# Kernel tuning notes

Hardware: AMD Instinct MI355X
Metric: run time of the kernel (lower is better)

## Reference

```python
import jax, jax.numpy as jnp
import numpy as np
import math

B, T, H, NH, L = 8, 256, 128, 2, 2
DH = H // NH
KC = 3
ITEMNUM = 50000
TIME_SPAN = 256
PERIODS = jnp.array([86400.0, 604800.0, 2592000.0], dtype=jnp.float32)
SCALE_MAGS = [1.0, 1.0, 1.0]
NEG = -1e9


def layernorm(x, g, b, eps=1e-8):
    mu = x.mean(-1, keepdims=True)
    var = ((x - mu) ** 2).mean(-1, keepdims=True)
    return (x - mu) / jnp.sqrt(var + eps) * g + b


def time_encode(t, time_proj):
    # HarmonicTimeEncoding: [sin(2*pi*t/c), cos(2*pi*t/c)] per cycle -> Linear(2K->H, no bias)
    phase = 2.0 * math.pi * t[..., None] / PERIODS
    enc = jnp.concatenate([jnp.sin(phase), jnp.cos(phase)], axis=-1)  # (..., 2K)
    return enc @ time_proj.T


def phase_bias_fn(t, lambdas):
    # PhaseSimilarityBias: per-cycle cosine similarity of (sin,cos) phase vectors
    phase = 2.0 * math.pi * t[..., None] / PERIODS  # (B,T,K)
    phi = jnp.stack([jnp.sin(phase), jnp.cos(phase)], axis=-1)  # (B,T,K,2)
    phi = phi / jnp.maximum(jnp.linalg.norm(phi, axis=-1, keepdims=True), 1e-12)
    sim = jnp.einsum('btkd,bskd->btsk', phi, phi)
    return (sim * lambdas).sum(-1)  # (B,T,T)


def setup_inputs() -> dict:
    key = jax.random.key(0)
    ks = jax.random.split(key, 40)
    def n(i, shape, std=0.02):
        return jax.random.normal(ks[i], shape, dtype=jnp.float32) * std
    inp = {}
    inp['log_seqs'] = jax.random.randint(ks[0], (B, T), 0, ITEMNUM + 1)
    inp['time_matrices'] = jax.random.randint(ks[1], (B, T, T), 0, TIME_SPAN + 1)
    inp['time_seq'] = jnp.sort(jax.random.uniform(ks[2], (B, T), dtype=jnp.float32) * 5e6, axis=-1)
    inp['pos_seqs'] = jax.random.randint(ks[3], (B, T), 1, ITEMNUM + 1)
    inp['neg_seqs'] = jax.random.randint(ks[4], (B, T), 1, ITEMNUM + 1)
    inp['target_times'] = jax.random.uniform(ks[5], (B,), dtype=jnp.float32) * 5e6
    inp['item_emb'] = n(6, (ITEMNUM + 1, H)).at[0].set(0.0)  # padding_idx=0
    inp['abs_pos_K'] = n(7, (T, H))
    inp['abs_pos_V'] = n(8, (T, H))
    inp['time_K_emb'] = n(9, (TIME_SPAN + 1, H))
    inp['time_V_emb'] = n(10, (TIME_SPAN + 1, H))
    inp['Wq'] = n(11, (L, H, H), 0.05); inp['bq'] = jnp.zeros((L, H))
    inp['Wk'] = n(12, (L, H, H), 0.05); inp['bk'] = jnp.zeros((L, H))
    inp['Wv'] = n(13, (L, H, H), 0.05); inp['bv'] = jnp.zeros((L, H))
    inp['attn_ln_g'] = jnp.ones((L, H)); inp['attn_ln_b'] = jnp.zeros((L, H))
    inp['fwd_ln_g'] = jnp.ones((L, H)); inp['fwd_ln_b'] = jnp.zeros((L, H))
    inp['w1'] = n(14, (L, H, H), 0.05); inp['b1'] = jnp.zeros((L, H))
    inp['w2'] = n(15, (L, H, H), 0.05); inp['b2'] = jnp.zeros((L, H))
    inp['last_ln_g'] = jnp.ones((H,)); inp['last_ln_b'] = jnp.zeros((H,))
    inp['time_proj'] = n(16, (H, 2 * KC), 1.0 / math.sqrt(H))
    inp['lambdas'] = jnp.array(SCALE_MAGS, dtype=jnp.float32)
    inp['pred_W'] = n(17, (H, H), 0.05)
    inp['fus_W1'] = n(18, (H, 2 * H), 0.05); inp['fus_b1'] = jnp.zeros((H,))
    inp['fus_W2'] = n(19, (H, H), 0.05); inp['fus_b2'] = jnp.zeros((H,))
    return inp


def reference(log_seqs, time_matrices, time_seq, pos_seqs, neg_seqs, target_times,
              item_emb, abs_pos_K, abs_pos_V, time_K_emb, time_V_emb,
              Wq, bq, Wk, bk, Wv, bv, attn_ln_g, attn_ln_b, fwd_ln_g, fwd_ln_b,
              w1, b1, w2, b2, last_ln_g, last_ln_b, time_proj, lambdas,
              pred_W, fus_W1, fus_b1, fus_W2, fus_b2):
    seqs = item_emb[log_seqs] * math.sqrt(H)
    seqs = seqs + time_encode(time_seq, time_proj)
    tl_mask = (log_seqs == 0)  # (B,T) padding mask
    keep = (~tl_mask)[..., None].astype(seqs.dtype)
    seqs = seqs * keep
    absK = abs_pos_K.reshape(T, NH, DH).transpose(1, 0, 2)  # (NH,T,DH)
    absV = abs_pos_V.reshape(T, NH, DH).transpose(1, 0, 2)
    tK = time_K_emb[time_matrices].reshape(B, T, T, NH, DH)  # (B,T,T,NH,DH)
    tV = time_V_emb[time_matrices].reshape(B, T, T, NH, DH)
    pbias = phase_bias_fn(time_seq, lambdas)  # (B,T,T)
    causal = jnp.triu(jnp.ones((T, T), dtype=bool), k=1)
    mask = causal[None, None] | tl_mask[:, None, None, :]  # (B,1,T,T)
    for l in range(L):
        Qn = layernorm(seqs, attn_ln_g[l], attn_ln_b[l])
        q = (Qn @ Wq[l].T + bq[l]).reshape(B, T, NH, DH).transpose(0, 2, 1, 3)
        k = (seqs @ Wk[l].T + bk[l]).reshape(B, T, NH, DH).transpose(0, 2, 1, 3)
        v = (seqs @ Wv[l].T + bv[l]).reshape(B, T, NH, DH).transpose(0, 2, 1, 3)
        scores = jnp.einsum('bhqd,bhkd->bhqk', q, k)
        scores = scores + jnp.einsum('bhqd,hkd->bhqk', q, absK)
        scores = scores + jnp.einsum('bqkhd,bhqd->bhqk', tK, q)  # relative time-interval term
        scores = scores / math.sqrt(DH) + pbias[:, None]  # phase-similarity logit bias
        scores = jnp.where(mask, NEG, scores)
        A = jax.nn.softmax(scores, axis=-1)
        out = jnp.einsum('bhqk,bhkd->bhqd', A, v)
        out = out + jnp.einsum('bhqk,hkd->bhqd', A, absV)
        out = out + jnp.einsum('bhqk,bqkhd->bhqd', A, tV)
        out = out.transpose(0, 2, 1, 3).reshape(B, T, H)
        seqs = Qn + out
        x = layernorm(seqs, fwd_ln_g[l], fwd_ln_b[l])
        seqs = jax.nn.relu(x @ w1[l].T + b1[l]) @ w2[l].T + b2[l] + x
        seqs = seqs * keep
    log_feats = layernorm(seqs, last_ln_g, last_ln_b)
    H_per = time_encode(target_times, time_proj) @ pred_W.T  # (B,H)
    H_per = jnp.broadcast_to(H_per[:, None], (B, T, H))
    cat = jnp.concatenate([log_feats, H_per], axis=-1)
    fused = jax.nn.gelu(cat @ fus_W1.T + fus_b1, approximate=False) @ fus_W2.T + fus_b2
    pos_logits = (fused * item_emb[pos_seqs]).sum(-1)
    neg_logits = (fused * item_emb[neg_seqs]).sum(-1)
    return (pos_logits, neg_logits)
```

## Files before the change

kernel.cpp:

```cpp
#include <hip/hip_runtime.h>
#include <math.h>

#define TT 256
#define HH 128

__device__ __forceinline__ void enc6(float t, float e[6]) {
  float x = 6.2831853071795864769f * t;
  float a0 = x / 86400.0f, a1 = x / 604800.0f, a2 = x / 2592000.0f;
  e[0] = sinf(a0); e[1] = sinf(a1); e[2] = sinf(a2);
  e[3] = cosf(a0); e[4] = cosf(a1); e[5] = cosf(a2);
}

__global__ __launch_bounds__(128) void embed_kernel(
    const int* __restrict__ log_seqs, const float* __restrict__ time_seq,
    const float* __restrict__ item_emb, const float* __restrict__ time_proj,
    float* __restrict__ seqs, float* __restrict__ sc6) {
  int row = blockIdx.x;
  int h = threadIdx.x;
  float t = time_seq[row];
  float e[6]; enc6(t, e);
  int idx = log_seqs[row];
  const float* tp = time_proj + h * 6;
  float val = item_emb[(size_t)idx * HH + h] * 11.313708498984761f;
  val += e[0]*tp[0] + e[1]*tp[1] + e[2]*tp[2] + e[3]*tp[3] + e[4]*tp[4] + e[5]*tp[5];
  seqs[(size_t)row * HH + h] = (idx != 0) ? val : 0.0f;
  if (h < 6) sc6[row * 6 + h] = e[h];
}

__global__ __launch_bounds__(128) void qkv_fused(
    const float* __restrict__ S,
    const float* __restrict__ Wq, const float* __restrict__ bq,
    const float* __restrict__ Wk, const float* __restrict__ bk,
    const float* __restrict__ Wv, const float* __restrict__ bv,
    const float* __restrict__ lng, const float* __restrict__ lnb,
    const float* __restrict__ absK, const float* __restrict__ absV,
    float* __restrict__ QN, float* __restrict__ QB,
    float* __restrict__ KT, float* __restrict__ VB) {
  int which = blockIdx.x >> 8;
  int m0 = (blockIdx.x & 255) * 8;
  int n = threadIdx.x;
  __shared__ float At[8][132];
  __shared__ float mu[8], rs[8];
  #pragma unroll
  for (int r = 0; r < 8; ++r) At[r][n] = S[(size_t)(m0 + r) * HH + n];
  __syncthreads();
  if (which == 0) {
    if (n < 64) {
      int r = n >> 3, sg = n & 7;
      float s = 0.f;
      #pragma unroll
      for (int i = 0; i < 16; ++i) s += At[r][sg * 16 + i];
      s += __shfl_xor(s, 1); s += __shfl_xor(s, 2); s += __shfl_xor(s, 4);
      if (sg == 0) mu[r] = s * (1.0f / HH);
    }
    __syncthreads();
    if (n < 64) {
      int r = n >> 3, sg = n & 7;
      float mm = mu[r], s = 0.f;
      #pragma unroll
      for (int i = 0; i < 16; ++i) { float d = At[r][sg*16+i] - mm; s += d * d; }
      s += __shfl_xor(s, 1); s += __shfl_xor(s, 2); s += __shfl_xor(s, 4);
      if (sg == 0) rs[r] = rsqrtf(s * (1.0f / HH) + 1e-8f);
    }
    __syncthreads();
    float gg = lng[n], bb = lnb[n];
    #pragma unroll
    for (int r = 0; r < 8; ++r) {
      float v = (At[r][n] - mu[r]) * rs[r] * gg + bb;
      At[r][n] = v;
      QN[(size_t)(m0 + r) * HH + n] = v;
    }
    __syncthreads();
  }
  const float* W    = which == 0 ? Wq : which == 1 ? Wk : Wv;
  const float* bias = which == 0 ? bq : which == 1 ? bk : bv;
  const float* addP = which == 1 ? absK : which == 2 ? absV : nullptr;
  float* dst        = which == 0 ? QB : which == 1 ? KT : VB;
  float acc[8];
  #pragma unroll
  for (int r = 0; r < 8; ++r) acc[r] = 0.f;
  const float* wr = W + (size_t)n * HH;
  for (int d = 0; d < HH; d += 4) {
    float4 w = *(const float4*)(wr + d);
    #pragma unroll
    for (int r = 0; r < 8; ++r) {
      float4 a = *(const float4*)(&At[r][d]);
      acc[r] = fmaf(a.x, w.x, fmaf(a.y, w.y, fmaf(a.z, w.z, fmaf(a.w, w.w, acc[r]))));
    }
  }
  float bn = bias[n];
  #pragma unroll
  for (int r = 0; r < 8; ++r) {
    int m = m0 + r;
    float v = acc[r] + bn;
    if (addP) v += addP[(size_t)(m & 255) * HH + n];
    if (which == 1) {
      int bb2 = m >> 8, t = m & 255, hh2 = n >> 6, dd = n & 63;
      dst[(((size_t)(bb2 * 2 + hh2) * 64) + dd) * 256 + t] = v;
    } else {
      dst[(size_t)m * HH + n] = v;
    }
  }
}

__global__ __launch_bounds__(256) void pkscb_kernel(
    const float* __restrict__ QB, const float* __restrict__ tKe,
    const int* __restrict__ tmat, const int* __restrict__ log_seqs,
    const float* __restrict__ sc6, const float* __restrict__ lambdas,
    float* __restrict__ SCB) {
  int blk = blockIdx.x;
  int qt = blk & 63, bh = blk >> 6;
  int h = bh & 1, b = bh >> 1;
  int q0 = qt << 2, hoff = h << 6;
  int tid = threadIdx.x;
  __shared__ float Qs[4][64];
  __shared__ float PKl[4][264];
  __shared__ float sk6T[6][256];
  __shared__ float sq6[4][6];
  __shared__ unsigned char kmask[256];
  { int q = tid >> 6, d = tid & 63;
    Qs[q][d] = QB[((size_t)(b * TT + q0 + q)) * HH + hoff + d]; }
  for (int idx = tid; idx < 1536; idx += 256) {
    int kk = idx / 6, cc = idx - kk * 6;
    sk6T[cc][kk] = sc6[(size_t)b * 1536 + idx];
  }
  if (tid < 24) {
    int q = tid / 6, cc = tid - q * 6;
    sq6[q][cc] = sc6[((size_t)(b * TT + q0 + q)) * 6 + cc];
  }
  kmask[tid] = (log_seqs[b * TT + tid] == 0) ? 1 : 0;
  __syncthreads();
  for (int i = tid; i < 257; i += 256) {
    const float* tp = tKe + (size_t)i * HH + hoff;
    float a0 = 0.f, a1 = 0.f, a2 = 0.f, a3 = 0.f;
    #pragma unroll
    for (int d = 0; d < 64; d += 4) {
      float4 t4 = *(const float4*)(tp + d);
      float4 v0 = *(const float4*)(&Qs[0][d]);
      float4 v1 = *(const float4*)(&Qs[1][d]);
      float4 v2 = *(const float4*)(&Qs[2][d]);
      float4 v3 = *(const float4*)(&Qs[3][d]);
      a0 = fmaf(v0.x,t4.x,fmaf(v0.y,t4.y,fmaf(v0.z,t4.z,fmaf(v0.w,t4.w,a0))));
      a1 = fmaf(v1.x,t4.x,fmaf(v1.y,t4.y,fmaf(v1.z,t4.z,fmaf(v1.w,t4.w,a1))));
      a2 = fmaf(v2.x,t4.x,fmaf(v2.y,t4.y,fmaf(v2.z,t4.z,fmaf(v2.w,t4.w,a2))));
      a3 = fmaf(v3.x,t4.x,fmaf(v3.y,t4.y,fmaf(v3.z,t4.z,fmaf(v3.w,t4.w,a3))));
    }
    PKl[0][i] = a0 * 0.125f; PKl[1][i] = a1 * 0.125f;
    PKl[2][i] = a2 * 0.125f; PKl[3][i] = a3 * 0.125f;
  }
  __syncthreads();
  float l0 = lambdas[0], l1 = lambdas[1], l2 = lambdas[2];
  int k = tid;
  float c0 = sk6T[0][k], c1 = sk6T[1][k], c2 = sk6T[2][k],
        c3 = sk6T[3][k], c4 = sk6T[4][k], c5 = sk6T[5][k];
  int km = kmask[k];
  float* scbq = SCB + ((size_t)(bh * TT + q0)) * TT;
  #pragma unroll
  for (int qq = 0; qq < 4; ++qq) {
    int qg = q0 + qq;
    float pb = l0 * (sq6[qq][0] * c0 + sq6[qq][3] * c3)
             + l1 * (sq6[qq][1] * c1 + sq6[qq][4] * c4)
             + l2 * (sq6[qq][2] * c2 + sq6[qq][5] * c5);
    int tm = tmat[((size_t)(b * TT + qg)) * TT + k];
    float val = (k > qg || km) ? -1e9f : (PKl[qq][tm] + pb);
    scbq[(size_t)qq * TT + k] = val;
  }
}

__global__ __launch_bounds__(256) void attn_fused(
    const float* __restrict__ QB, const float* __restrict__ KT,
    const float* __restrict__ VB, const float* __restrict__ QN,
    const float* __restrict__ SCB, const int* __restrict__ tmat,
    const float* __restrict__ tVe, float* __restrict__ out) {
  int blk = blockIdx.x;
  blk = (blk & 7) * 256 + (blk >> 3);
  int qt = blk & 127;
  int h = (blk >> 7) & 1;
  int b = blk >> 8;
  int q0 = qt << 1;
  int hoff = h << 6;
  int tid = threadIdx.x;
  int w = tid >> 6, lane = tid & 63;

  __shared__ float Qt[2][64];
  __shared__ float Pp[2][256];
  __shared__ unsigned short tmq[2][256];
  __shared__ float part[4][2][64];
  __shared__ float red[16];

  if (tid < 128)
    Qt[tid >> 6][tid & 63] = QB[((size_t)(b * TT + q0 + (tid >> 6))) * HH + hoff + (tid & 63)];
  #pragma unroll
  for (int t = 0; t < 2; ++t) {
    int idx = tid + t * 256;
    int qq = idx >> 8, kk = idx & 255;
    tmq[qq][kk] = (unsigned short)tmat[((size_t)(b * TT + q0 + qq)) * TT + kk];
  }
  __syncthreads();

  int k = (w << 6) | lane;
  const float* scb0 = SCB + ((size_t)((b * 2 + h) * TT + q0)) * TT;
  float s0 = scb0[k];
  float s1 = scb0[TT + k];
  if ((w << 6) <= q0 + 1) {
    float a0 = 0.f, a1 = 0.f;
    const float* ktb = KT + ((size_t)((b * 2 + h) * 64)) * 256 + k;
    #pragma unroll
    for (int d4 = 0; d4 < 16; ++d4) {
      float4 qa = *(const float4*)(&Qt[0][d4 << 2]);
      float4 qb = *(const float4*)(&Qt[1][d4 << 2]);
      const float* kp = ktb + (size_t)(d4 << 2) * 256;
      float v0 = kp[0], v1 = kp[256], v2 = kp[512], v3 = kp[768];
      a0 = fmaf(qa.x, v0, fmaf(qa.y, v1, fmaf(qa.z, v2, fmaf(qa.w, v3, a0))));
      a1 = fmaf(qb.x, v0, fmaf(qb.y, v1, fmaf(qb.z, v2, fmaf(qb.w, v3, a1))));
    }
    if (s0 > -5e8f) s0 = fmaf(a0, 0.125f, s0);
    if (s1 > -5e8f) s1 = fmaf(a1, 0.125f, s1);
  }
  float m0 = s0, m1 = s1;
  #pragma unroll
  for (int o = 32; o > 0; o >>= 1) {
    m0 = fmaxf(m0, __shfl_xor(m0, o));
    m1 = fmaxf(m1, __shfl_xor(m1, o));
  }
  if (lane == 0) { red[w] = m0; red[4 + w] = m1; }
  __syncthreads();
  float gm0 = fmaxf(fmaxf(red[0], red[1]), fmaxf(red[2], red[3]));
  float gm1 = fmaxf(fmaxf(red[4], red[5]), fmaxf(red[6], red[7]));
  float p0 = (gm0 < -5e8f) ? 1.0f : __expf(s0 - gm0);
  float p1 = (gm1 < -5e8f) ? 1.0f : __expf(s1 - gm1);
  float u0 = p0, u1 = p1;
  #pragma unroll
  for (int o = 32; o > 0; o >>= 1) {
    u0 += __shfl_xor(u0, o);
    u1 += __shfl_xor(u1, o);
  }
  if (lane == 0) { red[8 + w] = u0; red[12 + w] = u1; }
  __syncthreads();
  float inv0 = 1.0f / (red[8] + red[9] + red[10] + red[11]);
  float inv1 = 1.0f / (red[12] + red[13] + red[14] + red[15]);
  Pp[0][k] = p0 * inv0;
  Pp[1][k] = p1 * inv1;
  __syncthreads();

  int kend = (gm0 < -5e8f || gm1 < -5e8f) ? 256 : (q0 + 2);
  float o0 = 0.f, o1 = 0.f;
  const float* vbase = VB + ((size_t)(b * TT)) * HH + hoff + lane;
  const float* tvb   = tVe + hoff + lane;
  for (int kk = w; kk < kend; kk += 4) {
    float pa  = Pp[0][kk];
    float pb2 = Pp[1][kk];
    int ta = tmq[0][kk], tb = tmq[1][kk];
    float v  = vbase[(size_t)kk * HH];
    float t0 = tvb[(size_t)ta * HH];
    float t1 = tvb[(size_t)tb * HH];
    o0 = fmaf(pa,  v + t0, o0);
    o1 = fmaf(pb2, v + t1, o1);
  }
  part[w][0][lane] = o0;
  part[w][1][lane] = o1;
  __syncthreads();
  if (tid < 128) {
    int qq = tid >> 6, d = tid & 63;
    float o = part[0][qq][d] + part[1][qq][d] + part[2][qq][d] + part[3][qq][d];
    size_t ob = ((size_t)(b * TT + q0 + qq)) * HH + hoff + d;
    out[ob] = QN[ob] + o;
  }
}

__global__ __launch_bounds__(128) void ffn_fused(
    const float* __restrict__ S, const float* __restrict__ W1, const float* __restrict__ b1,
    const float* __restrict__ W2, const float* __restrict__ b2,
    const float* __restrict__ lng, const float* __restrict__ lnb,
    const int* __restrict__ log_seqs, float* __restrict__ outS) {
  int m0 = blockIdx.x * 4;
  int n = threadIdx.x;
  __shared__ float Xt[4][132];
  __shared__ float Ht[4][132];
  __shared__ float mu[4], rs[4];
  #pragma unroll
  for (int r = 0; r < 4; ++r) Xt[r][n] = S[(size_t)(m0 + r) * HH + n];
  __syncthreads();
  if (n < 32) {
    int r = n >> 3, sg = n & 7;
    float s = 0.f;
    #pragma unroll
    for (int i = 0; i < 16; ++i) s += Xt[r][sg * 16 + i];
    s += __shfl_xor(s, 1); s += __shfl_xor(s, 2); s += __shfl_xor(s, 4);
    if (sg == 0) mu[r] = s * (1.0f / HH);
  }
  __syncthreads();
  if (n < 32) {
    int r = n >> 3, sg = n & 7;
    float mm = mu[r], s = 0.f;
    #pragma unroll
    for (int i = 0; i < 16; ++i) { float d = Xt[r][sg*16+i] - mm; s += d * d; }
    s += __shfl_xor(s, 1); s += __shfl_xor(s, 2); s += __shfl_xor(s, 4);
    if (sg == 0) rs[r] = rsqrtf(s * (1.0f / HH) + 1e-8f);
  }
  __syncthreads();
  float gg = lng[n], bb = lnb[n];
  #pragma unroll
  for (int r = 0; r < 4; ++r) Xt[r][n] = (Xt[r][n] - mu[r]) * rs[r] * gg + bb;
  __syncthreads();
  float acc[4] = {0.f, 0.f, 0.f, 0.f};
  const float* wr = W1 + (size_t)n * HH;
  for (int d = 0; d < HH; d += 4) {
    float4 w = *(const float4*)(wr + d);
    #pragma unroll
    for (int r = 0; r < 4; ++r) {
      float4 a = *(const float4*)(&Xt[r][d]);
      acc[r] = fmaf(a.x, w.x, fmaf(a.y, w.y, fmaf(a.z, w.z, fmaf(a.w, w.w, acc[r]))));
    }
  }
  float b1n = b1[n];
  #pragma unroll
  for (int r = 0; r < 4; ++r) Ht[r][n] = fmaxf(acc[r] + b1n, 0.f);
  __syncthreads();
  float acc2[4] = {0.f, 0.f, 0.f, 0.f};
  wr = W2 + (size_t)n * HH;
  for (int d = 0; d < HH; d += 4) {
    float4 w = *(const float4*)(wr + d);
    #pragma unroll
    for (int r = 0; r < 4; ++r) {
      float4 a = *(const float4*)(&Ht[r][d]);
      acc2[r] = fmaf(a.x, w.x, fmaf(a.y, w.y, fmaf(a.z, w.z, fmaf(a.w, w.w, acc2[r]))));
    }
  }
  float b2n = b2[n];
  #pragma unroll
  for (int r = 0; r < 4; ++r) {
    int mrow = m0 + r;
    float v = acc2[r] + b2n + Xt[r][n];
    if (log_seqs[mrow] == 0) v = 0.f;
    outS[(size_t)mrow * HH + n] = v;
  }
}

__global__ __launch_bounds__(128) void hper_kernel(
    const float* __restrict__ target_t, const float* __restrict__ time_proj,
    const float* __restrict__ pred_W, const float* __restrict__ fus_W1,
    const float* __restrict__ fus_b1, float* __restrict__ hp1) {
  int b = blockIdx.x, hth = threadIdx.x;
  __shared__ float te[HH], hp[HH];
  float e[6]; enc6(target_t[b], e);
  const float* tp = time_proj + hth * 6;
  te[hth] = e[0]*tp[0]+e[1]*tp[1]+e[2]*tp[2]+e[3]*tp[3]+e[4]*tp[4]+e[5]*tp[5];
  __syncthreads();
  float u = 0.f;
  const float* pw = pred_W + (size_t)hth * HH;
  for (int d = 0; d < HH; ++d) u += te[d] * pw[d];
  hp[hth] = u;
  __syncthreads();
  float w = fus_b1[hth];
  const float* f1 = fus_W1 + (size_t)hth * 256 + 128;
  for (int d = 0; d < HH; ++d) w += hp[d] * f1[d];
  hp1[b * HH + hth] = w;
}

__global__ __launch_bounds__(128) void final_fused(
    const float* __restrict__ S, const float* __restrict__ lng, const float* __restrict__ lnb,
    const float* __restrict__ fus_W1, const float* __restrict__ HP1,
    const float* __restrict__ fus_W2, const float* __restrict__ fus_b2,
    const float* __restrict__ item_emb, const int* __restrict__ pos,
    const int* __restrict__ neg, float* __restrict__ out) {
  int m0 = blockIdx.x * 4;
  int bidx = m0 >> 8;
  int n = threadIdx.x;
  __shared__ float Xt[4][132];
  __shared__ float Ht[4][132];
  __shared__ float Ft[4][132];
  __shared__ float mu[4], rs[4];
  #pragma unroll
  for (int r = 0; r < 4; ++r) Xt[r][n] = S[(size_t)(m0 + r) * HH + n];
  __syncthreads();
  if (n < 32) {
    int r = n >> 3, sg = n & 7;
    float s = 0.f;
    #pragma unroll
    for (int i = 0; i < 16; ++i) s += Xt[r][sg * 16 + i];
    s += __shfl_xor(s, 1); s += __shfl_xor(s, 2); s += __shfl_xor(s, 4);
    if (sg == 0) mu[r] = s * (1.0f / HH);
  }
  __syncthreads();
  if (n < 32) {
    int r = n >> 3, sg = n & 7;
    float mm = mu[r], s = 0.f;
    #pragma unroll
    for (int i = 0; i < 16; ++i) { float d = Xt[r][sg*16+i] - mm; s += d * d; }
    s += __shfl_xor(s, 1); s += __shfl_xor(s, 2); s += __shfl_xor(s, 4);
    if (sg == 0) rs[r] = rsqrtf(s * (1.0f / HH) + 1e-8f);
  }
  __syncthreads();
  float gg = lng[n], bb = lnb[n];
  #pragma unroll
  for (int r = 0; r < 4; ++r) Xt[r][n] = (Xt[r][n] - mu[r]) * rs[r] * gg + bb;
  __syncthreads();
  float acc[4] = {0.f, 0.f, 0.f, 0.f};
  const float* wr = fus_W1 + (size_t)n * 256;
  for (int d = 0; d < HH; d += 4) {
    float4 w = *(const float4*)(wr + d);
    #pragma unroll
    for (int r = 0; r < 4; ++r) {
      float4 a = *(const float4*)(&Xt[r][d]);
      acc[r] = fmaf(a.x, w.x, fmaf(a.y, w.y, fmaf(a.z, w.z, fmaf(a.w, w.w, acc[r]))));
    }
  }
  float hp = HP1[bidx * HH + n];
  #pragma unroll
  for (int r = 0; r < 4; ++r) {
    float v = acc[r] + hp;
    Ht[r][n] = 0.5f * v * (1.0f + erff(v * 0.70710678118654752f));
  }
  __syncthreads();
  float acc2[4] = {0.f, 0.f, 0.f, 0.f};
  wr = fus_W2 + (size_t)n * HH;
  for (int d = 0; d < HH; d += 4) {
    float4 w = *(const float4*)(wr + d);
    #pragma unroll
    for (int r = 0; r < 4; ++r) {
      float4 a = *(const float4*)(&Ht[r][d]);
      acc2[r] = fmaf(a.x, w.x, fmaf(a.y, w.y, fmaf(a.z, w.z, fmaf(a.w, w.w, acc2[r]))));
    }
  }
  float b2n = fus_b2[n];
  #pragma unroll
  for (int r = 0; r < 4; ++r) Ft[r][n] = acc2[r] + b2n;
  __syncthreads();
  if (n < 64) {
    int task = n >> 3;
    int sg = n & 7;
    int r = task & 3;
    int w = task >> 2;
    int mrow = m0 + r;
    int idx = (w == 0) ? pos[mrow] : neg[mrow];
    const float* ie = item_emb + (size_t)idx * HH;
    float s = 0.f;
    #pragma unroll
    for (int i = 0; i < 16; ++i) s += Ft[r][sg * 16 + i] * ie[sg * 16 + i];
    s += __shfl_xor(s, 1); s += __shfl_xor(s, 2); s += __shfl_xor(s, 4);
    if (sg == 0) out[w * 2048 + mrow] = s;
  }
}

extern "C" void kernel_launch(void* const* d_in, const int* in_sizes, int n_in,
                              void* d_out, int out_size, void* d_ws, size_t ws_size,
                              hipStream_t stream) {
  const int*   log_seqs   = (const int*)d_in[0];
  const int*   tmat       = (const int*)d_in[1];
  const float* time_seq   = (const float*)d_in[2];
  const int*   pos_seqs   = (const int*)d_in[3];
  const int*   neg_seqs   = (const int*)d_in[4];
  const float* target_t   = (const float*)d_in[5];
  const float* item_emb   = (const float*)d_in[6];
  const float* abs_pos_K  = (const float*)d_in[7];
  const float* abs_pos_V  = (const float*)d_in[8];
  const float* time_K_emb = (const float*)d_in[9];
  const float* time_V_emb = (const float*)d_in[10];
  const float* Wq = (const float*)d_in[11];
  const float* bq = (const float*)d_in[12];
  const float* Wk = (const float*)d_in[13];
  const float* bk = (const float*)d_in[14];
  const float* Wv = (const float*)d_in[15];
  const float* bv = (const float*)d_in[16];
  const float* attn_ln_g = (const float*)d_in[17];
  const float* attn_ln_b = (const float*)d_in[18];
  const float* fwd_ln_g = (const float*)d_in[19];
  const float* fwd_ln_b = (const float*)d_in[20];
  const float* w1 = (const float*)d_in[21];
  const float* b1 = (const float*)d_in[22];
  const float* w2 = (const float*)d_in[23];
  const float* b2 = (const float*)d_in[24];
  const float* last_ln_g = (const float*)d_in[25];
  const float* last_ln_b = (const float*)d_in[26];
  const float* time_proj = (const float*)d_in[27];
  const float* lambdas = (const float*)d_in[28];
  const float* pred_W = (const float*)d_in[29];
  const float* fus_W1 = (const float*)d_in[30];
  const float* fus_b1 = (const float*)d_in[31];
  const float* fus_W2 = (const float*)d_in[32];
  const float* fus_b2 = (const float*)d_in[33];
  (void)in_sizes; (void)n_in; (void)out_size; (void)ws_size;

  float* out = (float*)d_out;
  float* ws = (float*)d_ws;
  const int M = 8 * TT;
  float* SC6  = ws;
  float* SEQS = SC6 + M * 6;
  float* QN   = SEQS + M * HH;
  float* QB   = QN + M * HH;
  float* KT   = QB + M * HH;
  float* VB   = KT + M * HH;
  float* HP1  = VB + M * HH;
  float* SCB  = HP1 + 8 * HH;

  embed_kernel<<<M, HH, 0, stream>>>(log_seqs, time_seq, item_emb, time_proj, SEQS, SC6);
  for (int l = 0; l < 2; ++l) {
    const size_t wo = (size_t)l * HH * HH;
    const size_t bo = (size_t)l * HH;
    qkv_fused<<<768, 128, 0, stream>>>(SEQS, Wq + wo, bq + bo, Wk + wo, bk + bo,
                                       Wv + wo, bv + bo, attn_ln_g + bo, attn_ln_b + bo,
                                       abs_pos_K, abs_pos_V, QN, QB, KT, VB);
    pkscb_kernel<<<1024, 256, 0, stream>>>(QB, time_K_emb, tmat, log_seqs, SC6, lambdas, SCB);
    attn_fused<<<2048, 256, 0, stream>>>(QB, KT, VB, QN, SCB, tmat, time_V_emb, SEQS);
    ffn_fused<<<512, 128, 0, stream>>>(SEQS, w1 + wo, b1 + bo, w2 + wo, b2 + bo,
                                       fwd_ln_g + bo, fwd_ln_b + bo, log_seqs, SEQS);
  }
  hper_kernel<<<8, 128, 0, stream>>>(target_t, time_proj, pred_W, fus_W1, fus_b1, HP1);
  final_fused<<<512, 128, 0, stream>>>(SEQS, last_ln_g, last_ln_b, fus_W1, HP1,
                                       fus_W2, fus_b2, item_emb, pos_seqs, neg_seqs, out);
}
```

Measured before the change: 294.5 us.

## Fuse score-bias kernel into attention and merge hper into embed kernel

Removes the separate pkscb kernel and its SCB score buffer (B*NH*T*T floats written then read each layer). Attention now computes the time-key, phase-bias and mask terms in-block, handling four queries per block with per-warp softmax. The hper kernel is folded into the embed launch as extra blocks, and qkv blocks shrink from 8 to 4 rows to launch more blocks. This cuts launches and global traffic, but each attention block now redoes the time-key projection over 257 entries for its 4 queries.

```diff
diff --git a/kernel.cpp b/kernel.cpp
--- a/kernel.cpp
+++ b/kernel.cpp
@@ -11,20 +11,40 @@
   e[3] = cosf(a0); e[4] = cosf(a1); e[5] = cosf(a2);
 }
 
-__global__ __launch_bounds__(128) void embed_kernel(
+__global__ __launch_bounds__(128) void embed_hper_kernel(
     const int* __restrict__ log_seqs, const float* __restrict__ time_seq,
     const float* __restrict__ item_emb, const float* __restrict__ time_proj,
-    float* __restrict__ seqs, float* __restrict__ sc6) {
-  int row = blockIdx.x;
-  int h = threadIdx.x;
-  float t = time_seq[row];
-  float e[6]; enc6(t, e);
-  int idx = log_seqs[row];
-  const float* tp = time_proj + h * 6;
-  float val = item_emb[(size_t)idx * HH + h] * 11.313708498984761f;
-  val += e[0]*tp[0] + e[1]*tp[1] + e[2]*tp[2] + e[3]*tp[3] + e[4]*tp[4] + e[5]*tp[5];
-  seqs[(size_t)row * HH + h] = (idx != 0) ? val : 0.0f;
-  if (h < 6) sc6[row * 6 + h] = e[h];
+    const float* __restrict__ target_t, const float* __restrict__ pred_W,
+    const float* __restrict__ fus_W1, const float* __restrict__ fus_b1,
+    float* __restrict__ seqs, float* __restrict__ sc6, float* __restrict__ hp1) {
+  int blk = blockIdx.x;
+  int tid = threadIdx.x;
+  if (blk < 2048) {
+    float t = time_seq[blk];
+    float e[6]; enc6(t, e);
+    int idx = log_seqs[blk];
+    const float* tp = time_proj + tid * 6;
+    float val = item_emb[(size_t)idx * HH + tid] * 11.313708498984761f;
+    val += e[0]*tp[0] + e[1]*tp[1] + e[2]*tp[2] + e[3]*tp[3] + e[4]*tp[4] + e[5]*tp[5];
+    seqs[(size_t)blk * HH + tid] = (idx != 0) ? val : 0.0f;
+    if (tid < 6) sc6[blk * 6 + tid] = e[tid];
+  } else {
+    int b = blk - 2048;
+    __shared__ float te[HH], hp[HH];
+    float e[6]; enc6(target_t[b], e);
+    const float* tp = time_proj + tid * 6;
+    te[tid] = e[0]*tp[0]+e[1]*tp[1]+e[2]*tp[2]+e[3]*tp[3]+e[4]*tp[4]+e[5]*tp[5];
+    __syncthreads();
+    float u = 0.f;
+    const float* pw = pred_W + (size_t)tid * HH;
+    for (int d = 0; d < HH; ++d) u += te[d] * pw[d];
+    hp[tid] = u;
+    __syncthreads();
+    float w = fus_b1[tid];
+    const float* f1 = fus_W1 + (size_t)tid * 256 + 128;
+    for (int d = 0; d < HH; ++d) w += hp[d] * f1[d];
+    hp1[b * HH + tid] = w;
+  }
 }
 
 __global__ __launch_bounds__(128) void qkv_fused(
@@ -36,16 +56,16 @@
     const float* __restrict__ absK, const float* __restrict__ absV,
     float* __restrict__ QN, float* __restrict__ QB,
     float* __restrict__ KT, float* __restrict__ VB) {
-  int which = blockIdx.x >> 8;
-  int m0 = (blockIdx.x & 255) * 8;
+  int which = blockIdx.x >> 9;
+  int m0 = (blockIdx.x & 511) * 4;
   int n = threadIdx.x;
-  __shared__ float At[8][132];
-  __shared__ float mu[8], rs[8];
-  #pragma unroll
-  for (int r = 0; r < 8; ++r) At[r][n] = S[(size_t)(m0 + r) * HH + n];
+  __shared__ float At[4][132];
+  __shared__ float mu[4], rs[4];
+  #pragma unroll
+  for (int r = 0; r < 4; ++r) At[r][n] = S[(size_t)(m0 + r) * HH + n];
   __syncthreads();
   if (which == 0) {
-    if (n < 64) {
+    if (n < 32) {
       int r = n >> 3, sg = n & 7;
       float s = 0.f;
       #pragma unroll
@@ -54,7 +74,7 @@
       if (sg == 0) mu[r] = s * (1.0f / HH);
     }
     __syncthreads();
-    if (n < 64) {
+    if (n < 32) {
       int r = n >> 3, sg = n & 7;
       float mm = mu[r], s = 0.f;
       #pragma unroll
@@ -65,7 +85,7 @@
     __syncthreads();
     float gg = lng[n], bb = lnb[n];
     #pragma unroll
-    for (int r = 0; r < 8; ++r) {
+    for (int r = 0; r < 4; ++r) {
       float v = (At[r][n] - mu[r]) * rs[r] * gg + bb;
       At[r][n] = v;
       QN[(size_t)(m0 + r) * HH + n] = v;
@@ -76,21 +96,19 @@
   const float* bias = which == 0 ? bq : which == 1 ? bk : bv;
   const float* addP = which == 1 ? absK : which == 2 ? absV : nullptr;
   float* dst        = which == 0 ? QB : which == 1 ? KT : VB;
-  float acc[8];
-  #pragma unroll
-  for (int r = 0; r < 8; ++r) acc[r] = 0.f;
+  float acc[4] = {0.f, 0.f, 0.f, 0.f};
   const float* wr = W + (size_t)n * HH;
   for (int d = 0; d < HH; d += 4) {
     float4 w = *(const float4*)(wr + d);
     #pragma unroll
-    for (int r = 0; r < 8; ++r) {
+    for (int r = 0; r < 4; ++r) {
       float4 a = *(const float4*)(&At[r][d]);
       acc[r] = fmaf(a.x, w.x, fmaf(a.y, w.y, fmaf(a.z, w.z, fmaf(a.w, w.w, acc[r]))));
     }
   }
   float bn = bias[n];
   #pragma unroll
-  for (int r = 0; r < 8; ++r) {
+  for (int r = 0; r < 4; ++r) {
     int m = m0 + r;
     float v = acc[r] + bn;
     if (addP) v += addP[(size_t)(m & 255) * HH + n];
@@ -103,21 +121,33 @@
   }
 }
 
-__global__ __launch_bounds__(256) void pkscb_kernel(
-    const float* __restrict__ QB, const float* __restrict__ tKe,
-    const int* __restrict__ tmat, const int* __restrict__ log_seqs,
-    const float* __restrict__ sc6, const float* __restrict__ lambdas,
-    float* __restrict__ SCB) {
+__global__ __launch_bounds__(256) void attn_fused(
+    const float* __restrict__ QB, const float* __restrict__ KT,
+    const float* __restrict__ VB, const float* __restrict__ QN,
+    const int* __restrict__ log_seqs, const int* __restrict__ tmat,
+    const float* __restrict__ sc6, const float* __restrict__ tKe,
+    const float* __restrict__ tVe, const float* __restrict__ lambdas,
+    float* __restrict__ out) {
   int blk = blockIdx.x;
-  int qt = blk & 63, bh = blk >> 6;
-  int h = bh & 1, b = bh >> 1;
-  int q0 = qt << 2, hoff = h << 6;
+  blk = (blk & 7) * 128 + (blk >> 3);
+  int qt = blk & 63;
+  int h = (blk >> 6) & 1;
+  int b = blk >> 7;
+  int q0 = qt << 2;
+  int hoff = h << 6;
   int tid = threadIdx.x;
+  int w = tid >> 6, lane = tid & 63;
+
   __shared__ float Qs[4][64];
-  __shared__ float PKl[4][264];
+  __shared__ float PKs[4][260];
   __shared__ float sk6T[6][256];
-  __shared__ float sq6[4][6];
+  __shared__ float sq6v[4][6];
+  __shared__ unsigned short tmq[4][256];
   __shared__ unsigned char kmask[256];
+  __shared__ float Pp[4][256];
+  __shared__ float part[4][4][64];
+  __shared__ float redm[4];
+
   { int q = tid >> 6, d = tid & 63;
     Qs[q][d] = QB[((size_t)(b * TT + q0 + q)) * HH + hoff + d]; }
   for (int idx = tid; idx < 1536; idx += 256) {
@@ -126,10 +156,17 @@
   }
   if (tid < 24) {
     int q = tid / 6, cc = tid - q * 6;
-    sq6[q][cc] = sc6[((size_t)(b * TT + q0 + q)) * 6 + cc];
+    sq6v[q][cc] = sc6[((size_t)(b * TT + q0 + q)) * 6 + cc];
+  }
+  #pragma unroll
+  for (int t = 0; t < 4; ++t) {
+    int idx = tid + (t << 8);
+    int qq = idx >> 8, kk = idx & 255;
+    tmq[qq][kk] = (unsigned short)tmat[((size_t)(b * TT + q0 + qq)) * TT + kk];
   }
   kmask[tid] = (log_seqs[b * TT + tid] == 0) ? 1 : 0;
   __syncthreads();
+
   for (int i = tid; i < 257; i += 256) {
     const float* tp = tKe + (size_t)i * HH + hoff;
     float a0 = 0.f, a1 = 0.f, a2 = 0.f, a3 = 0.f;
@@ -145,127 +182,100 @@
       a2 = fmaf(v2.x,t4.x,fmaf(v2.y,t4.y,fmaf(v2.z,t4.z,fmaf(v2.w,t4.w,a2))));
       a3 = fmaf(v3.x,t4.x,fmaf(v3.y,t4.y,fmaf(v3.z,t4.z,fmaf(v3.w,t4.w,a3))));
     }
-    PKl[0][i] = a0 * 0.125f; PKl[1][i] = a1 * 0.125f;
-    PKl[2][i] = a2 * 0.125f; PKl[3][i] = a3 * 0.125f;
-  }
-  __syncthreads();
-  float l0 = lambdas[0], l1 = lambdas[1], l2 = lambdas[2];
+    PKs[0][i] = a0 * 0.125f; PKs[1][i] = a1 * 0.125f;
+    PKs[2][i] = a2 * 0.125f; PKs[3][i] = a3 * 0.125f;
+  }
+  __syncthreads();
+
   int k = tid;
-  float c0 = sk6T[0][k], c1 = sk6T[1][k], c2 = sk6T[2][k],
-        c3 = sk6T[3][k], c4 = sk6T[4][k], c5 = sk6T[5][k];
-  int km = kmask[k];
-  float* scbq = SCB + ((size_t)(bh * TT + q0)) * TT;
-  #pragma unroll
-  for (int qq = 0; qq < 4; ++qq) {
-    int qg = q0 + qq;
-    float pb = l0 * (sq6[qq][0] * c0 + sq6[qq][3] * c3)
-             + l1 * (sq6[qq][1] * c1 + sq6[qq][4] * c4)
-             + l2 * (sq6[qq][2] * c2 + sq6[qq][5] * c5);
-    int tm = tmat[((size_t)(b * TT + qg)) * TT + k];
-    float val = (k > qg || km) ? -1e9f : (PKl[qq][tm] + pb);
-    scbq[(size_t)qq * TT + k] = val;
-  }
-}
-
-__global__ __launch_bounds__(256) void attn_fused(
-    const float* __restrict__ QB, const float* __restrict__ KT,
-    const float* __restrict__ VB, const float* __restrict__ QN,
-    const float* __restrict__ SCB, const int* __restrict__ tmat,
-    const float* __restrict__ tVe, float* __restrict__ out) {
-  int blk = blockIdx.x;
-  blk = (blk & 7) * 256 + (blk >> 3);
-  int qt = blk & 127;
-  int h = (blk >> 7) & 1;
-  int b = blk >> 8;
-  int q0 = qt << 1;
-  int hoff = h << 6;
-  int tid = threadIdx.x;
-  int w = tid >> 6, lane = tid & 63;
-
-  __shared__ float Qt[2][64];
-  __shared__ float Pp[2][256];
-  __shared__ unsigned short tmq[2][256];
-  __shared__ float part[4][2][64];
-  __shared__ float red[16];
-
-  if (tid < 128)
-    Qt[tid >> 6][tid & 63] = QB[((size_t)(b * TT + q0 + (tid >> 6))) * HH + hoff + (tid & 63)];
-  #pragma unroll
-  for (int t = 0; t < 2; ++t) {
-    int idx = tid + t * 256;
-    int qq = idx >> 8, kk = idx & 255;
-    tmq[qq][kk] = (unsigned short)tmat[((size_t)(b * TT + q0 + qq)) * TT + kk];
-  }
-  __syncthreads();
-
-  int k = (w << 6) | lane;
-  const float* scb0 = SCB + ((size_t)((b * 2 + h) * TT + q0)) * TT;
-  float s0 = scb0[k];
-  float s1 = scb0[TT + k];
-  if ((w << 6) <= q0 + 1) {
-    float a0 = 0.f, a1 = 0.f;
-    const float* ktb = KT + ((size_t)((b * 2 + h) * 64)) * 256 + k;
-    #pragma unroll
-    for (int d4 = 0; d4 < 16; ++d4) {
-      float4 qa = *(const float4*)(&Qt[0][d4 << 2]);
-      float4 qb = *(const float4*)(&Qt[1][d4 << 2]);
-      const float* kp = ktb + (size_t)(d4 << 2) * 256;
-      float v0 = kp[0], v1 = kp[256], v2 = kp[512], v3 = kp[768];
-      a0 = fmaf(qa.x, v0, fmaf(qa.y, v1, fmaf(qa.z, v2, fmaf(qa.w, v3, a0))));
-      a1 = fmaf(qb.x, v0, fmaf(qb.y, v1, fmaf(qb.z, v2, fmaf(qb.w, v3, a1))));
-    }
-    if (s0 > -5e8f) s0 = fmaf(a0, 0.125f, s0);
-    if (s1 > -5e8f) s1 = fmaf(a1, 0.125f, s1);
-  }
-  float m0 = s0, m1 = s1;
-  #pragma unroll
-  for (int o = 32; o > 0; o >>= 1) {
-    m0 = fmaxf(m0, __shfl_xor(m0, o));
-    m1 = fmaxf(m1, __shfl_xor(m1, o));
-  }
-  if (lane == 0) { red[w] = m0; red[4 + w] = m1; }
-  __syncthreads();
-  float gm0 = fmaxf(fmaxf(red[0], red[1]), fmaxf(red[2], red[3]));
-  float gm1 = fmaxf(fmaxf(red[4], red[5]), fmaxf(red[6], red[7]));
-  float p0 = (gm0 < -5e8f) ? 1.0f : __expf(s0 - gm0);
-  float p1 = (gm1 < -5e8f) ? 1.0f : __expf(s1 - gm1);
-  float u0 = p0, u1 = p1;
-  #pragma unroll
-  for (int o = 32; o > 0; o >>= 1) {
-    u0 += __shfl_xor(u0, o);
-    u1 += __shfl_xor(u1, o);
-  }
-  if (lane == 0) { red[8 + w] = u0; red[12 + w] = u1; }
-  __syncthreads();
-  float inv0 = 1.0f / (red[8] + red[9] + red[10] + red[11]);
-  float inv1 = 1.0f / (red[12] + red[13] + red[14] + red[15]);
-  Pp[0][k] = p0 * inv0;
-  Pp[1][k] = p1 * inv1;
-  __syncthreads();
-
-  int kend = (gm0 < -5e8f || gm1 < -5e8f) ? 256 : (q0 + 2);
-  float o0 = 0.f, o1 = 0.f;
+  {
+    float d0 = 0.f, d1 = 0.f, d2 = 0.f, d3 = 0.f;
+    if (k <= q0 + 3) {
+      const float* ktc = KT + ((size_t)((b * 2 + h) * 64)) * 256 + k;
+      #pragma unroll
+      for (int d4 = 0; d4 < 16; ++d4) {
+        float4 qa = *(const float4*)(&Qs[0][d4 << 2]);
+        float4 qb = *(const float4*)(&Qs[1][d4 << 2]);
+        float4 qc = *(const float4*)(&Qs[2][d4 << 2]);
+        float4 qd = *(const float4*)(&Qs[3][d4 << 2]);
+        float v0 = ktc[(size_t)((d4 << 2) + 0) * 256];
+        float v1 = ktc[(size_t)((d4 << 2) + 1) * 256];
+        float v2 = ktc[(size_t)((d4 << 2) + 2) * 256];
+        float v3 = ktc[(size_t)((d4 << 2) + 3) * 256];
+        d0 = fmaf(qa.x, v0, fmaf(qa.y, v1, fmaf(qa.z, v2, fmaf(qa.w, v3, d0))));
+        d1 = fmaf(qb.x, v0, fmaf(qb.y, v1, fmaf(qb.z, v2, fmaf(qb.w, v3, d1))));
+        d2 = fmaf(qc.x, v0, fmaf(qc.y, v1, fmaf(qc.z, v2, fmaf(qc.w, v3, d2))));
+        d3 = fmaf(qd.x, v0, fmaf(qd.y, v1, fmaf(qd.z, v2, fmaf(qd.w, v3, d3))));
+      }
+    }
+    float dq[4] = {d0, d1, d2, d3};
+    float l0 = lambdas[0], l1 = lambdas[1], l2 = lambdas[2];
+    float c0 = sk6T[0][k], c1 = sk6T[1][k], c2 = sk6T[2][k],
+          c3 = sk6T[3][k], c4 = sk6T[4][k], c5 = sk6T[5][k];
+    int km = kmask[k];
+    #pragma unroll
+    for (int qq = 0; qq < 4; ++qq) {
+      int qg = q0 + qq;
+      float sv = -1e9f;
+      if (k <= qg && !km) {
+        float pb = l0 * (sq6v[qq][0] * c0 + sq6v[qq][3] * c3)
+                 + l1 * (sq6v[qq][1] * c1 + sq6v[qq][4] * c4)
+                 + l2 * (sq6v[qq][2] * c2 + sq6v[qq][5] * c5);
+        sv = fmaf(dq[qq], 0.125f, PKs[qq][tmq[qq][k]] + pb);
+      }
+      Pp[qq][k] = sv;
+    }
+  }
+  __syncthreads();
+
+  {
+    float s4[4];
+    #pragma unroll
+    for (int j = 0; j < 4; ++j) s4[j] = Pp[w][lane + (j << 6)];
+    float mx = fmaxf(fmaxf(s4[0], s4[1]), fmaxf(s4[2], s4[3]));
+    #pragma unroll
+    for (int o = 32; o > 0; o >>= 1) mx = fmaxf(mx, __shfl_xor(mx, o));
+    bool full = (mx < -5e8f);
+    float p[4], sum = 0.f;
+    #pragma unroll
+    for (int j = 0; j < 4; ++j) { p[j] = full ? 1.0f : __expf(s4[j] - mx); sum += p[j]; }
+    #pragma unroll
+    for (int o = 32; o > 0; o >>= 1) sum += __shfl_xor(sum, o);
+    float inv = 1.0f / sum;
+    #pragma unroll
+    for (int j = 0; j < 4; ++j) Pp[w][lane + (j << 6)] = p[j] * inv;
+    if (lane == 0) redm[w] = mx;
+  }
+  __syncthreads();
+
+  bool anyfull = (redm[0] < -5e8f) || (redm[1] < -5e8f) ||
+                 (redm[2] < -5e8f) || (redm[3] < -5e8f);
+  int kend = anyfull ? 256 : (q0 + 4);
+
+  float o0 = 0.f, o1 = 0.f, o2 = 0.f, o3 = 0.f;
   const float* vbase = VB + ((size_t)(b * TT)) * HH + hoff + lane;
   const float* tvb   = tVe + hoff + lane;
   for (int kk = w; kk < kend; kk += 4) {
-    float pa  = Pp[0][kk];
-    float pb2 = Pp[1][kk];
-    int ta = tmq[0][kk], tb = tmq[1][kk];
-    float v  = vbase[(size_t)kk * HH];
-    float t0 = tvb[(size_t)ta * HH];
-    float t1 = tvb[(size_t)tb * HH];
-    o0 = fmaf(pa,  v + t0, o0);
-    o1 = fmaf(pb2, v + t1, o1);
+    float v = vbase[(size_t)kk * HH];
+    float pA = Pp[0][kk], pB = Pp[1][kk], pC = Pp[2][kk], pD = Pp[3][kk];
+    float tA = tvb[(size_t)tmq[0][kk] * HH];
+    float tB = tvb[(size_t)tmq[1][kk] * HH];
+    float tC = tvb[(size_t)tmq[2][kk] * HH];
+    float tD = tvb[(size_t)tmq[3][kk] * HH];
+    o0 = fmaf(pA, v + tA, o0);
+    o1 = fmaf(pB, v + tB, o1);
+    o2 = fmaf(pC, v + tC, o2);
+    o3 = fmaf(pD, v + tD, o3);
   }
   part[w][0][lane] = o0;
   part[w][1][lane] = o1;
-  __syncthreads();
-  if (tid < 128) {
-    int qq = tid >> 6, d = tid & 63;
+  part[w][2][lane] = o2;
+  part[w][3][lane] = o3;
+  __syncthreads();
+  { int qq = tid >> 6, d = tid & 63;
     float o = part[0][qq][d] + part[1][qq][d] + part[2][qq][d] + part[3][qq][d];
     size_t ob = ((size_t)(b * TT + q0 + qq)) * HH + hoff + d;
-    out[ob] = QN[ob] + o;
-  }
+    out[ob] = QN[ob] + o; }
 }
 
 __global__ __launch_bounds__(128) void ffn_fused(
@@ -335,27 +345,6 @@
     if (log_seqs[mrow] == 0) v = 0.f;
     outS[(size_t)mrow * HH + n] = v;
   }
-}
-
-__global__ __launch_bounds__(128) void hper_kernel(
-    const float* __restrict__ target_t, const float* __restrict__ time_proj,
-    const float* __restrict__ pred_W, const float* __restrict__ fus_W1,
-    const float* __restrict__ fus_b1, float* __restrict__ hp1) {
-  int b = blockIdx.x, hth = threadIdx.x;
-  __shared__ float te[HH], hp[HH];
-  float e[6]; enc6(target_t[b], e);
-  const float* tp = time_proj + hth * 6;
-  te[hth] = e[0]*tp[0]+e[1]*tp[1]+e[2]*tp[2]+e[3]*tp[3]+e[4]*tp[4]+e[5]*tp[5];
-  __syncthreads();
-  float u = 0.f;
-  const float* pw = pred_W + (size_t)hth * HH;
-  for (int d = 0; d < HH; ++d) u += te[d] * pw[d];
-  hp[hth] = u;
-  __syncthreads();
-  float w = fus_b1[hth];
-  const float* f1 = fus_W1 + (size_t)hth * 256 + 128;
-  for (int d = 0; d < HH; ++d) w += hp[d] * f1[d];
-  hp1[b * HH + hth] = w;
 }
 
 __global__ __launch_bounds__(128) void final_fused(
@@ -492,21 +481,21 @@
   float* KT   = QB + M * HH;
   float* VB   = KT + M * HH;
   float* HP1  = VB + M * HH;
-  float* SCB  = HP1 + 8 * HH;
-
-  embed_kernel<<<M, HH, 0, stream>>>(log_seqs, time_seq, item_emb, time_proj, SEQS, SC6);
+
+  embed_hper_kernel<<<2056, 128, 0, stream>>>(log_seqs, time_seq, item_emb, time_proj,
+                                              target_t, pred_W, fus_W1, fus_b1,
+                                              SEQS, SC6, HP1);
   for (int l = 0; l < 2; ++l) {
     const size_t wo = (size_t)l * HH * HH;
     const size_t bo = (size_t)l * HH;
-    qkv_fused<<<768, 128, 0, stream>>>(SEQS, Wq + wo, bq + bo, Wk + wo, bk + bo,
-                                       Wv + wo, bv + bo, attn_ln_g + bo, attn_ln_b + bo,
-                                       abs_pos_K, abs_pos_V, QN, QB, KT, VB);
-    pkscb_kernel<<<1024, 256, 0, stream>>>(QB, time_K_emb, tmat, log_seqs, SC6, lambdas, SCB);
-    attn_fused<<<2048, 256, 0, stream>>>(QB, KT, VB, QN, SCB, tmat, time_V_emb, SEQS);
+    qkv_fused<<<1536, 128, 0, stream>>>(SEQS, Wq + wo, bq + bo, Wk + wo, bk + bo,
+                                        Wv + wo, bv + bo, attn_ln_g + bo, attn_ln_b + bo,
+                                        abs_pos_K, abs_pos_V, QN, QB, KT, VB);
+    attn_fused<<<1024, 256, 0, stream>>>(QB, KT, VB, QN, log_seqs, tmat, SC6,
+                                         time_K_emb, time_V_emb, lambdas, SEQS);
     ffn_fused<<<512, 128, 0, stream>>>(SEQS, w1 + wo, b1 + bo, w2 + wo, b2 + bo,
                                        fwd_ln_g + bo, fwd_ln_b + bo, log_seqs, SEQS);
   }
-  hper_kernel<<<8, 128, 0, stream>>>(target_t, time_proj, pred_W, fus_W1, fus_b1, HP1);
   final_fused<<<512, 128, 0, stream>>>(SEQS, last_ln_g, last_ln_b, fus_W1, HP1,
                                        fus_W2, fus_b2, item_emb, pos_seqs, neg_seqs, out);
 }
```

After: 299.9 us. About the same (+1.8%).
